# Kernel tuning notes

Hardware: AMD Instinct MI355X
Metric: run time of the kernel (lower is better)

Reference implementation:

```python
import jax, jax.numpy as jnp
import numpy as np

N, E, G = 40000, 640000, 64
D, H, O = 128, 128, 10
EPS = 1e-5


def _lin(k, fan_in, shape):
    b = 1.0 / np.sqrt(fan_in)
    return jax.random.uniform(k, shape, jnp.float32, -b, b)


def setup_inputs() -> dict:
    key = jax.random.key(0)
    ks = jax.random.split(key, 12)
    x = jax.random.normal(ks[0], (N, D), jnp.float32)
    edge_index = jax.random.randint(ks[1], (2, E), 0, N)
    batch = jnp.sort(jax.random.randint(ks[2], (N,), 0, G))
    return {
        "x": x,
        "edge_index": edge_index,
        "batch": batch,
        "num_graphs": G,
        "W_gcn": _lin(ks[3], D, (D, H)),
        "b_gcn": jnp.zeros((H,), jnp.float32),
        "gamma": jnp.ones((H,), jnp.float32),
        "beta": jnp.zeros((H,), jnp.float32),
        "W1": _lin(ks[4], 3 * H, (3 * H, H)),
        "b1": _lin(ks[5], 3 * H, (H,)),
        "W2": _lin(ks[6], H, (H, H // 2)),
        "b2": _lin(ks[7], H, (H // 2,)),
        "W3": _lin(ks[8], H // 2, (H // 2, O)),
        "b3": _lin(ks[9], H // 2, (O,)),
    }


def reference(x, edge_index, batch, num_graphs, W_gcn, b_gcn, gamma, beta, W1, b1, W2, b2, W3, b3):
    n = x.shape[0]
    src, dst = edge_index[0], edge_index[1]
    # GCNConv: h = D^{-1/2} (A + I) D^{-1/2} (x W) + b  (self-loops, symmetric norm)
    h = x @ W_gcn                                   # [N, H]
    deg = jax.ops.segment_sum(jnp.ones((src.shape[0],), h.dtype), dst, num_segments=n) + 1.0
    dinv = jax.lax.rsqrt(deg)                       # [N]
    coef = dinv[src] * dinv[dst]                    # [E]
    msg = h[src] * coef[:, None]                    # [E, H] gather (memory bound)
    agg = jax.ops.segment_sum(msg, dst, num_segments=n)
    agg = agg + h * (dinv * dinv)[:, None] + b_gcn  # self-loop term + bias
    h = jax.nn.relu(agg)
    # LayerNorm over feature dim
    mu = jnp.mean(h, axis=-1, keepdims=True)
    var = jnp.mean(jnp.square(h - mu), axis=-1, keepdims=True)
    h = (h - mu) * jax.lax.rsqrt(var + EPS) * gamma + beta
    # global mean / add / max pools keyed by graph id
    counts = jax.ops.segment_sum(jnp.ones((n,), h.dtype), batch, num_segments=num_graphs)
    x_add = jax.ops.segment_sum(h, batch, num_segments=num_graphs)
    x_mean = x_add / jnp.maximum(counts, 1.0)[:, None]
    x_max = jax.ops.segment_max(h, batch, num_segments=num_graphs)
    x_max = jnp.where(counts[:, None] > 0, x_max, 0.0)
    g = jnp.concatenate([x_mean, x_add, x_max], axis=1)  # [G, 3H]
    # MLP head (dropout is identity at inference)
    g = jax.nn.relu(g @ W1 + b1)
    g = jax.nn.relu(g @ W2 + b2)
    return g @ W3 + b3
```

## Files before the change

### kernel.cpp

```cpp
#include <hip/hip_runtime.h>
#include <math.h>

#define EPS 1e-5f
#define FLT_BIG 3.402823466e38f

typedef __attribute__((ext_vector_type(8))) short bf16x8;
typedef __attribute__((ext_vector_type(4))) float f32x4;

__device__ __forceinline__ unsigned fflip(float f){
  int i = __float_as_int(f);
  return (unsigned)(i ^ ((i>>31) | 0x80000000));
}
__device__ __forceinline__ float funflip(unsigned u){
  int i = (u & 0x80000000u) ? (int)(u ^ 0x80000000u) : (int)(~u);
  return __int_as_float(i);
}
__device__ __forceinline__ unsigned f2bf(float f){
  unsigned u = __float_as_uint(f);
  return (u + 0x7FFFu + ((u>>16)&1u)) >> 16;
}
__device__ __forceinline__ float bf_lo(unsigned v){ return __uint_as_float(v<<16); }
__device__ __forceinline__ float bf_hi(unsigned v){ return __uint_as_float(v & 0xFFFF0000u); }

__device__ __forceinline__ int lbound(const int* __restrict__ a, int n, int key){
  int lo=0, hi=n;
  while(lo<hi){ int mid=(lo+hi)>>1; if(a[mid]<key) lo=mid+1; else hi=mid; }
  return lo;
}

__global__ __launch_bounds__(256) void k_bucketize(
    const int* __restrict__ src, const int* __restrict__ dst, int E, int NB,
    unsigned* __restrict__ gcur, unsigned* __restrict__ dstream,
    const float* __restrict__ Wg, ushort* __restrict__ Wp,
    const int* __restrict__ batch, int N, int* __restrict__ gcnt, int G){
  __shared__ unsigned whist[4][160];
  __shared__ unsigned hist[160];
  __shared__ unsigned excl[160];
  __shared__ unsigned base[160];
  __shared__ unsigned wsum[4];
  __shared__ unsigned lsorted[2048];
  int t = threadIdx.x, bid = blockIdx.x;
  int wid = t>>6, lane = t&63;

  if(bid < 8){
    int i = bid*256 + t;
    int tile = i>>6, l = i&63;
    int kt = tile>>3, ct = tile&7;
    int q = l>>4, nn = l&15;
    ushort w8[8];
    #pragma unroll
    for(int j=0;j<8;j++)
      w8[j] = (ushort)f2bf(Wg[(kt*32 + q*8 + j)*128 + ct*16 + nn]);
    ushort* dstp = Wp + (size_t)i*8;
    #pragma unroll
    for(int j=0;j<8;j++) dstp[j] = w8[j];
  } else if(bid == 8){
    if(t < G){
      int s = lbound(batch,N,t), e = lbound(batch,N,t+1);
      gcnt[t] = e - s;
    }
  }

  int e0 = bid*2048 + t*8;
  unsigned rec[8]; int bk[8]; unsigned rr[8];
  #pragma unroll
  for(int j=0;j<8;j++) bk[j] = -1;
  if(e0+7 < E){
    int4 s0 = *(const int4*)(src+e0), s1 = *(const int4*)(src+e0+4);
    int4 d0 = *(const int4*)(dst+e0), d1 = *(const int4*)(dst+e0+4);
    int ss[8] = {s0.x,s0.y,s0.z,s0.w,s1.x,s1.y,s1.z,s1.w};
    int dd[8] = {d0.x,d0.y,d0.z,d0.w,d1.x,d1.y,d1.z,d1.w};
    #pragma unroll
    for(int j=0;j<8;j++){
      bk[j] = dd[j]>>8;
      rec[j] = ((unsigned)bk[j]<<24) | ((unsigned)(dd[j]&255)<<16) | (unsigned)ss[j];
    }
  } else {
    #pragma unroll
    for(int j=0;j<8;j++){
      int ee = e0+j;
      if(ee<E){
        int s = src[ee], d = dst[ee];
        bk[j] = d>>8;
        rec[j] = ((unsigned)bk[j]<<24) | ((unsigned)(d&255)<<16) | (unsigned)s;
      }
    }
  }
  for(int i=t;i<NB;i+=256){
    whist[0][i]=0u; whist[1][i]=0u; whist[2][i]=0u; whist[3][i]=0u;
  }
  __syncthreads();
  #pragma unroll
  for(int j=0;j<8;j++)
    if(bk[j]>=0) rr[j] = atomicAdd(&whist[wid][bk[j]],1u);
  __syncthreads();
  unsigned hv = 0u;
  if(t<NB){
    unsigned h0=whist[0][t], h1=whist[1][t], h2=whist[2][t], h3=whist[3][t];
    hv = h0+h1+h2+h3;
    hist[t] = hv;
    whist[0][t]=0u; whist[1][t]=h0; whist[2][t]=h0+h1; whist[3][t]=h0+h1+h2;
  }
  unsigned v = hv;
  #pragma unroll
  for(int d=1; d<64; d<<=1){
    unsigned o = __shfl_up(v, d, 64);
    if(lane >= d) v += o;
  }
  if(lane==63) wsum[wid] = v;
  __syncthreads();
  {
    unsigned pre = 0;
    if(wid>0) pre += wsum[0];
    if(wid>1) pre += wsum[1];
    if(wid>2) pre += wsum[2];
    if(t<NB) excl[t] = v + pre - hv;
  }
  if(t<NB){
    int ridx = t + bid; while(ridx>=NB) ridx-=NB;
    base[ridx] = atomicAdd(&gcur[ridx], hist[ridx]);
  }
  __syncthreads();
  #pragma unroll
  for(int j=0;j<8;j++)
    if(bk[j]>=0) lsorted[excl[bk[j]] + whist[wid][bk[j]] + rr[j]] = rec[j];
  __syncthreads();
  int vc = E - bid*2048; if(vc>2048) vc=2048;
  #pragma unroll
  for(int j=0;j<8;j++){
    int k = j*256 + t;
    if(k<vc){
      unsigned rc = lsorted[k];
      unsigned bb = rc>>24;
      unsigned pos = base[bb] + (unsigned)k - excl[bb];
      if(pos < 8192u) dstream[((size_t)bb<<13) + pos] = rc;
    }
  }
}

__global__ __launch_bounds__(1024) void k_csrscale(
    const unsigned* __restrict__ dstream, const unsigned* __restrict__ gcur,
    int N, ushort* __restrict__ csr, int* __restrict__ cursor,
    const float4* __restrict__ x4, uint2* __restrict__ xs2){
  __shared__ unsigned cnt[256];
  __shared__ float dv[256];
  __shared__ ushort slab[16384];
  int b = blockIdx.x, t = threadIdx.x;
  if(t<256) cnt[t]=0u;
  {
    unsigned sv = ((unsigned)N<<16) | (unsigned)N;
    uint4 fillv = make_uint4(sv,sv,sv,sv);
    #pragma unroll
    for(int i=t;i<2048;i+=1024) ((uint4*)slab)[i] = fillv;
  }
  if(b==0 && t<16) ((uint4*)(xs2 + ((size_t)N<<5)))[t] = make_uint4(0,0,0,0);
  __syncthreads();
  int nb = (int)gcur[b]; if(nb>8192) nb=8192;
  const unsigned* sp = dstream + ((size_t)b<<13);
  for(int i=t;i<nb;i+=1024){
    unsigned rc = sp[i];
    int dl = (rc>>16)&255;
    unsigned p = atomicAdd(&cnt[dl],1u);
    if(p<64u) slab[(dl<<6)+(int)p] = (ushort)(rc & 0xFFFFu);
  }
  __syncthreads();
  const uint4* s4 = (const uint4*)slab;
  uint4* c4 = ((uint4*)csr) + ((size_t)b<<11);
  #pragma unroll
  for(int i=t;i<2048;i+=1024) c4[i] = s4[i];
  if(t<256){
    int node = (b<<8) + t;
    if(node<N) cursor[node] = (int)cnt[t];
    int deg = (int)cnt[t]; if(deg>64) deg=64;
    dv[t] = rsqrtf((float)deg + 1.0f);
  }
  __syncthreads();
  int base = b<<8;
  for(int i=t; i<8192; i+=1024){
    int nl = i>>5;
    int node = base + nl;
    if(node<N){
      float dinv = dv[nl];
      size_t idx = ((size_t)node<<5) + (i&31);
      float4 v = x4[idx];
      uint2 o;
      o.x = (f2bf(v.y*dinv)<<16) | f2bf(v.x*dinv);
      o.y = (f2bf(v.w*dinv)<<16) | f2bf(v.z*dinv);
      xs2[idx] = o;
    }
  }
}

__global__ void k_agg(const uint4* __restrict__ xs4, const int* __restrict__ cursor,
                      const ushort* __restrict__ csr, int n, uint4* __restrict__ zb4){
  int w = (blockIdx.x*blockDim.x + threadIdx.x)>>6;
  if(w>=n) return;
  int lane = threadIdx.x & 63;
  int grp = lane>>4, li = lane&15;
  int deg = cursor[w]; if(deg>64) deg=64;
  int k0 = w<<6;
  float dd = rsqrtf((float)deg + 1.0f);
  float a0=0.f,a1=0.f,a2=0.f,a3=0.f,a4=0.f,a5=0.f,a6=0.f,a7=0.f;
  if(grp==0){
    uint4 sv = xs4[(w<<4)+li];
    a0=bf_lo(sv.x); a1=bf_hi(sv.x); a2=bf_lo(sv.y); a3=bf_hi(sv.y);
    a4=bf_lo(sv.z); a5=bf_hi(sv.z); a6=bf_lo(sv.w); a7=bf_hi(sv.w);
  }
  for(int kb=0; kb<deg; kb+=16){
    int base = k0 + kb + (grp<<2);
    ushort4 s4 = *(const ushort4*)(csr + base);
    { uint4 v = xs4[((int)s4.x<<4)+li];
      a0+=bf_lo(v.x); a1+=bf_hi(v.x); a2+=bf_lo(v.y); a3+=bf_hi(v.y);
      a4+=bf_lo(v.z); a5+=bf_hi(v.z); a6+=bf_lo(v.w); a7+=bf_hi(v.w); }
    { uint4 v = xs4[((int)s4.y<<4)+li];
      a0+=bf_lo(v.x); a1+=bf_hi(v.x); a2+=bf_lo(v.y); a3+=bf_hi(v.y);
      a4+=bf_lo(v.z); a5+=bf_hi(v.z); a6+=bf_lo(v.w); a7+=bf_hi(v.w); }
    { uint4 v = xs4[((int)s4.z<<4)+li];
      a0+=bf_lo(v.x); a1+=bf_hi(v.x); a2+=bf_lo(v.y); a3+=bf_hi(v.y);
      a4+=bf_lo(v.z); a5+=bf_hi(v.z); a6+=bf_lo(v.w); a7+=bf_hi(v.w); }
    { uint4 v = xs4[((int)s4.w<<4)+li];
      a0+=bf_lo(v.x); a1+=bf_hi(v.x); a2+=bf_lo(v.y); a3+=bf_hi(v.y);
      a4+=bf_lo(v.z); a5+=bf_hi(v.z); a6+=bf_lo(v.w); a7+=bf_hi(v.w); }
  }
  a0 += __shfl_xor(a0,16,64); a1 += __shfl_xor(a1,16,64);
  a2 += __shfl_xor(a2,16,64); a3 += __shfl_xor(a3,16,64);
  a4 += __shfl_xor(a4,16,64); a5 += __shfl_xor(a5,16,64);
  a6 += __shfl_xor(a6,16,64); a7 += __shfl_xor(a7,16,64);
  a0 += __shfl_xor(a0,32,64); a1 += __shfl_xor(a1,32,64);
  a2 += __shfl_xor(a2,32,64); a3 += __shfl_xor(a3,32,64);
  a4 += __shfl_xor(a4,32,64); a5 += __shfl_xor(a5,32,64);
  a6 += __shfl_xor(a6,32,64); a7 += __shfl_xor(a7,32,64);
  if(grp==0){
    uint4 o;
    o.x = (f2bf(a1*dd)<<16) | f2bf(a0*dd);
    o.y = (f2bf(a3*dd)<<16) | f2bf(a2*dd);
    o.z = (f2bf(a5*dd)<<16) | f2bf(a4*dd);
    o.w = (f2bf(a7*dd)<<16) | f2bf(a6*dd);
    zb4[(w<<4)+li] = o;
  }
}

__global__ __launch_bounds__(256) void k_gemmln(
    const unsigned* __restrict__ zb, const ushort* __restrict__ Wp,
    const float* __restrict__ bgc, const float* __restrict__ gamma, const float* __restrict__ beta,
    const int* __restrict__ batch, int n,
    float* __restrict__ pool_sum, unsigned* __restrict__ pool_maxu){
  __shared__ float sred[4][128];
  __shared__ float mred[4][128];
  int t = threadIdx.x, lane = t & 63, wv = t >> 6;
  int rowBase = blockIdx.x*64;
  int q = lane>>4, nn = lane&15;
  int m = rowBase + wv*16 + nn;
  bf16x8 afr[4];
  if(m < n){
    const char* rp = (const char*)zb + (size_t)m*256;
    #pragma unroll
    for(int kt=0;kt<4;kt++)
      afr[kt] = *(const bf16x8*)(rp + kt*64 + q*16);
  } else {
    #pragma unroll
    for(int kt=0;kt<4;kt++) afr[kt] = (bf16x8){0,0,0,0,0,0,0,0};
  }

  f32x4 acc[8];
  #pragma unroll
  for(int ct=0;ct<8;ct++){
    f32x4 c = {0.f,0.f,0.f,0.f};
    #pragma unroll
    for(int kt=0;kt<4;kt++){
      bf16x8 bfr = *(const bf16x8*)(Wp + ((size_t)(kt*8+ct)*64 + lane)*8);
      c = __builtin_amdgcn_mfma_f32_16x16x32_bf16(afr[kt], bfr, c, 0, 0, 0);
    }
    acc[ct] = c;
  }
  float s[4]={0,0,0,0}, qq[4]={0,0,0,0};
  #pragma unroll
  for(int ct=0;ct<8;ct++){
    float bb = bgc[ct*16+nn];
    #pragma unroll
    for(int r=0;r<4;r++){
      float v = acc[ct][r] + bb;
      v = fmaxf(v, 0.f);
      acc[ct][r] = v;
      s[r] += v; qq[r] += v*v;
    }
  }
  #pragma unroll
  for(int d=1; d<16; d<<=1){
    #pragma unroll
    for(int r=0;r<4;r++){
      s[r]  += __shfl_xor(s[r],  d, 64);
      qq[r] += __shfl_xor(qq[r], d, 64);
    }
  }
  float mu[4], isd[4];
  #pragma unroll
  for(int r=0;r<4;r++){
    mu[r] = s[r]*(1.f/128.f);
    float var = qq[r]*(1.f/128.f) - mu[r]*mu[r];
    isd[r] = rsqrtf(var + EPS);
  }
  #pragma unroll
  for(int ct=0;ct<8;ct++){
    float gm = gamma[ct*16+nn], bt = beta[ct*16+nn];
    #pragma unroll
    for(int r=0;r<4;r++)
      acc[ct][r] = (acc[ct][r]-mu[r])*isd[r]*gm + bt;
  }
  int gbr[4];
  #pragma unroll
  for(int r=0;r<4;r++){
    int gr = rowBase + wv*16 + q*4 + r;
    gbr[r] = (gr < n) ? batch[gr] : -1;
  }
  int b0i = rowBase; if(b0i >= n) b0i = n-1;
  int b63i = rowBase + 63; if(b63i >= n) b63i = n-1;
  int gmin = batch[b0i], gmax = batch[b63i];
  if(gmax < gmin) gmax = gmin;
  for(int g=gmin; g<=gmax; ++g){
    #pragma unroll
    for(int ct=0;ct<8;ct++){
      float ssum = 0.f, smax = -FLT_BIG;
      #pragma unroll
      for(int r=0;r<4;r++){
        if(gbr[r]==g){
          ssum += acc[ct][r];
          smax = fmaxf(smax, acc[ct][r]);
        }
      }
      ssum += __shfl_xor(ssum, 16, 64);
      ssum += __shfl_xor(ssum, 32, 64);
      float o1 = __shfl_xor(smax, 16, 64); smax = fmaxf(smax, o1);
      float o2 = __shfl_xor(smax, 32, 64); smax = fmaxf(smax, o2);
      if(q==0){
        sred[wv][ct*16+nn] = ssum;
        mred[wv][ct*16+nn] = smax;
      }
    }
    __syncthreads();
    if(t < 128){
      float s0 = (sred[0][t]+sred[1][t]) + (sred[2][t]+sred[3][t]);
      float m0 = fmaxf(fmaxf(mred[0][t],mred[1][t]), fmaxf(mred[2][t],mred[3][t]));
      if(s0 != 0.f)    atomicAdd(&pool_sum[g*128 + t], s0);
      if(m0 > -FLT_BIG) atomicMax(&pool_maxu[g*128 + t], fflip(m0));
    }
    __syncthreads();
  }
}

__global__ __launch_bounds__(512) void k_head(
    const float* __restrict__ pool_sum, const unsigned* __restrict__ pool_maxu,
    const int* __restrict__ gcnt,
    const float* __restrict__ W1, const float* __restrict__ b1,
    const float* __restrict__ W2, const float* __restrict__ b2,
    const float* __restrict__ W3, const float* __restrict__ b3,
    float* __restrict__ out){
  int g = blockIdx.x, t = threadIdx.x;
  __shared__ float red[4][128];
  __shared__ float gl[384];
  __shared__ float h1[128];
  __shared__ float h2[64];
  int cnt = gcnt[g];
  if(t<384){
    int j = t & 127;
    if(t<128){
      gl[t] = pool_sum[g*128+j] / (float)((cnt>1)?cnt:1);
    } else if(t<256){
      gl[t] = pool_sum[g*128+j];
    } else {
      float m = funflip(pool_maxu[g*128+j]);
      gl[t] = (cnt>0) ? m : 0.f;
    }
  }
  __syncthreads();
  int j = t & 127, kh = t >> 7;
  float p=0.f;
  for(int k=kh*96; k<kh*96+96; k++) p += gl[k]*W1[k*128+j];
  red[kh][j]=p;
  __syncthreads();
  if(t<128){
    float v = red[0][t]+red[1][t]+red[2][t]+red[3][t]+b1[t];
    h1[t]=fmaxf(v,0.f);
  }
  __syncthreads();
  if(t<64){
    float a=b2[t];
    for(int k=0;k<128;k++) a += h1[k]*W2[k*64+t];
    h2[t]=fmaxf(a,0.f);
  }
  __syncthreads();
  if(t<10){
    float a=b3[t];
    for(int k=0;k<64;k++) a += h2[k]*W3[k*10+t];
    out[g*10+t]=a;
  }
}

extern "C" void kernel_launch(void* const* d_in, const int* in_sizes, int n_in,
                              void* d_out, int out_size, void* d_ws, size_t ws_size,
                              hipStream_t stream){
  const float* x     = (const float*)d_in[0];
  const int*   ei    = (const int*)d_in[1];
  const int*   batch = (const int*)d_in[2];
  const float* Wg    = (const float*)d_in[4];
  const float* bg    = (const float*)d_in[5];
  const float* gamma = (const float*)d_in[6];
  const float* beta  = (const float*)d_in[7];
  const float* W1    = (const float*)d_in[8];
  const float* b1    = (const float*)d_in[9];
  const float* W2    = (const float*)d_in[10];
  const float* b2    = (const float*)d_in[11];
  const float* W3    = (const float*)d_in[12];
  const float* b3    = (const float*)d_in[13];
  float* out = (float*)d_out;

  int N = in_sizes[0]/128;
  int E = in_sizes[1]/2;
  const int G = 64;
  const int* src = ei;
  const int* dst = ei + E;
  int NB = (N+255)>>8;

  char* p = (char*)d_ws;
  auto alloc=[&](size_t bytes)->char*{ char* r=p; p += (bytes+255)&~(size_t)255; return r; };
  size_t zr_bytes = (size_t)G*128*4 + (size_t)G*128*4 + 1024;
  char*     zr      = alloc(zr_bytes);
  float*    psum    = (float*)zr;
  unsigned* pmaxu   = (unsigned*)(zr + (size_t)G*128*4);
  unsigned* gcur    = (unsigned*)(zr + (size_t)G*128*4*2);
  int*      cursor  = (int*)     alloc((size_t)N*4);
  ushort*   csr     = (ushort*)  alloc((size_t)NB*16384*2);
  unsigned* zb      = (unsigned*)alloc((size_t)N*64*4);
  unsigned* xs      = (unsigned*)alloc((size_t)(N+1)*64*4);
  ushort*   Wp      = (ushort*)  alloc(2048*8*2);
  int*      gcnt    = (int*)     alloc((size_t)G*4);
  unsigned* dstream = (unsigned*)alloc((size_t)NB*8192*4);

  hipMemsetAsync(zr, 0, zr_bytes, stream);
  int bb = (E+2047)/2048;
  k_bucketize<<<bb,256,0,stream>>>(src,dst,E,NB,gcur,dstream,Wg,Wp,batch,N,gcnt,G);
  k_csrscale<<<NB,1024,0,stream>>>(dstream,gcur,N,csr,cursor,(const float4*)x,(uint2*)xs);
  int ab = (int)(((size_t)N*64 + 255)/256);
  k_agg<<<ab,256,0,stream>>>((const uint4*)xs,cursor,csr,N,(uint4*)zb);
  k_gemmln<<<(N+63)/64,256,0,stream>>>(zb,Wp,bg,gamma,beta,batch,N,psum,pmaxu);
  k_head<<<G,512,0,stream>>>(psum,pmaxu,gcnt,W1,b1,W2,b2,W3,b3,out);
}
```

Measured before the change: 156.8 us.

## Fuse MLP head into gemmln via last-block-per-graph completion counter

Removes the separate k_head launch. Each graph's pooled features are finalized by whichever gemmln block finishes last for that graph, which it detects with a per-graph atomic done counter and an expected block count computed in bucketize. That block then runs the three-layer MLP head in place. This saves one kernel launch and its tail, at the cost of extra shared memory and serial head work inside a few gemmln blocks. Correctness depends on gblk matching the gemmln loop's per-block graph iteration.

```diff
diff --git a/kernel.cpp b/kernel.cpp
--- a/kernel.cpp
+++ b/kernel.cpp
@@ -32,7 +32,8 @@
     const int* __restrict__ src, const int* __restrict__ dst, int E, int NB,
     unsigned* __restrict__ gcur, unsigned* __restrict__ dstream,
     const float* __restrict__ Wg, ushort* __restrict__ Wp,
-    const int* __restrict__ batch, int N, int* __restrict__ gcnt, int G){
+    const int* __restrict__ batch, int N, int* __restrict__ gcnt,
+    int* __restrict__ gblk, int G){
   __shared__ unsigned whist[4][160];
   __shared__ unsigned hist[160];
   __shared__ unsigned excl[160];
@@ -58,6 +59,7 @@
     if(t < G){
       int s = lbound(batch,N,t), e = lbound(batch,N,t+1);
       gcnt[t] = e - s;
+      gblk[t] = (e > s) ? (((e-1)>>6) - (s>>6) + 1) : 0;
     }
   }
 
@@ -244,9 +246,20 @@
     const unsigned* __restrict__ zb, const ushort* __restrict__ Wp,
     const float* __restrict__ bgc, const float* __restrict__ gamma, const float* __restrict__ beta,
     const int* __restrict__ batch, int n,
-    float* __restrict__ pool_sum, unsigned* __restrict__ pool_maxu){
+    float* __restrict__ pool_sum, unsigned* __restrict__ pool_maxu,
+    const int* __restrict__ gcnt, const int* __restrict__ gblk,
+    unsigned* __restrict__ gdone,
+    const float* __restrict__ W1, const float* __restrict__ b1,
+    const float* __restrict__ W2, const float* __restrict__ b2,
+    const float* __restrict__ W3, const float* __restrict__ b3,
+    float* __restrict__ out){
   __shared__ float sred[4][128];
   __shared__ float mred[4][128];
+  __shared__ float gl[384];
+  __shared__ float hred[2][128];
+  __shared__ float h1[128];
+  __shared__ float h2[64];
+  __shared__ int trig_s;
   int t = threadIdx.x, lane = t & 63, wv = t >> 6;
   int rowBase = blockIdx.x*64;
   int q = lane>>4, nn = lane&15;
@@ -345,54 +358,43 @@
       if(m0 > -FLT_BIG) atomicMax(&pool_maxu[g*128 + t], fflip(m0));
     }
     __syncthreads();
-  }
-}
-
-__global__ __launch_bounds__(512) void k_head(
-    const float* __restrict__ pool_sum, const unsigned* __restrict__ pool_maxu,
-    const int* __restrict__ gcnt,
-    const float* __restrict__ W1, const float* __restrict__ b1,
-    const float* __restrict__ W2, const float* __restrict__ b2,
-    const float* __restrict__ W3, const float* __restrict__ b3,
-    float* __restrict__ out){
-  int g = blockIdx.x, t = threadIdx.x;
-  __shared__ float red[4][128];
-  __shared__ float gl[384];
-  __shared__ float h1[128];
-  __shared__ float h2[64];
-  int cnt = gcnt[g];
-  if(t<384){
-    int j = t & 127;
-    if(t<128){
-      gl[t] = pool_sum[g*128+j] / (float)((cnt>1)?cnt:1);
-    } else if(t<256){
-      gl[t] = pool_sum[g*128+j];
-    } else {
-      float m = funflip(pool_maxu[g*128+j]);
-      gl[t] = (cnt>0) ? m : 0.f;
-    }
-  }
-  __syncthreads();
-  int j = t & 127, kh = t >> 7;
-  float p=0.f;
-  for(int k=kh*96; k<kh*96+96; k++) p += gl[k]*W1[k*128+j];
-  red[kh][j]=p;
-  __syncthreads();
-  if(t<128){
-    float v = red[0][t]+red[1][t]+red[2][t]+red[3][t]+b1[t];
-    h1[t]=fmaxf(v,0.f);
-  }
-  __syncthreads();
-  if(t<64){
-    float a=b2[t];
-    for(int k=0;k<128;k++) a += h1[k]*W2[k*64+t];
-    h2[t]=fmaxf(a,0.f);
-  }
-  __syncthreads();
-  if(t<10){
-    float a=b3[t];
-    for(int k=0;k<64;k++) a += h2[k]*W3[k*10+t];
-    out[g*10+t]=a;
+    if(t==0){
+      __threadfence();
+      unsigned old = atomicAdd(&gdone[g], 1u);
+      trig_s = (old == (unsigned)(gblk[g]-1));
+    }
+    __syncthreads();
+    if(trig_s){
+      int cnt = gcnt[g];
+      float rinv = 1.f/(float)((cnt>1)?cnt:1);
+      if(t<128){
+        float sv = atomicAdd(&pool_sum[g*128+t], 0.f);
+        gl[t]     = sv*rinv;
+        gl[128+t] = sv;
+        unsigned mu_ = atomicOr(&pool_maxu[g*128+t], 0u);
+        gl[256+t] = (cnt>0) ? funflip(mu_) : 0.f;
+      }
+      __syncthreads();
+      int j = t & 127, kh = t >> 7;
+      float p = 0.f;
+      for(int k=kh*192; k<kh*192+192; k++) p += gl[k]*W1[k*128+j];
+      hred[kh][j] = p;
+      __syncthreads();
+      if(t<128) h1[t] = fmaxf(hred[0][t]+hred[1][t]+b1[t], 0.f);
+      __syncthreads();
+      if(t<64){
+        float a = b2[t];
+        for(int k=0;k<128;k++) a += h1[k]*W2[k*64+t];
+        h2[t] = fmaxf(a, 0.f);
+      }
+      __syncthreads();
+      if(t<10){
+        float a = b3[t];
+        for(int k=0;k<64;k++) a += h2[k]*W3[k*10+t];
+        out[g*10+t] = a;
+      }
+    }
+    __syncthreads();
   }
 }
 
@@ -423,25 +425,27 @@
 
   char* p = (char*)d_ws;
   auto alloc=[&](size_t bytes)->char*{ char* r=p; p += (bytes+255)&~(size_t)255; return r; };
-  size_t zr_bytes = (size_t)G*128*4 + (size_t)G*128*4 + 1024;
+  size_t zr_bytes = (size_t)G*128*4*2 + 1024 + 1024;
   char*     zr      = alloc(zr_bytes);
   float*    psum    = (float*)zr;
   unsigned* pmaxu   = (unsigned*)(zr + (size_t)G*128*4);
   unsigned* gcur    = (unsigned*)(zr + (size_t)G*128*4*2);
+  unsigned* gdone   = (unsigned*)(zr + (size_t)G*128*4*2 + 1024);
   int*      cursor  = (int*)     alloc((size_t)N*4);
   ushort*   csr     = (ushort*)  alloc((size_t)NB*16384*2);
   unsigned* zb      = (unsigned*)alloc((size_t)N*64*4);
   unsigned* xs      = (unsigned*)alloc((size_t)(N+1)*64*4);
   ushort*   Wp      = (ushort*)  alloc(2048*8*2);
   int*      gcnt    = (int*)     alloc((size_t)G*4);
+  int*      gblk    = (int*)     alloc((size_t)G*4);
   unsigned* dstream = (unsigned*)alloc((size_t)NB*8192*4);
 
   hipMemsetAsync(zr, 0, zr_bytes, stream);
   int bb = (E+2047)/2048;
-  k_bucketize<<<bb,256,0,stream>>>(src,dst,E,NB,gcur,dstream,Wg,Wp,batch,N,gcnt,G);
+  k_bucketize<<<bb,256,0,stream>>>(src,dst,E,NB,gcur,dstream,Wg,Wp,batch,N,gcnt,gblk,G);
   k_csrscale<<<NB,1024,0,stream>>>(dstream,gcur,N,csr,cursor,(const float4*)x,(uint2*)xs);
   int ab = (int)(((size_t)N*64 + 255)/256);
   k_agg<<<ab,256,0,stream>>>((const uint4*)xs,cursor,csr,N,(uint4*)zb);
-  k_gemmln<<<(N+63)/64,256,0,stream>>>(zb,Wp,bg,gamma,beta,batch,N,psum,pmaxu);
-  k_head<<<G,512,0,stream>>>(psum,pmaxu,gcnt,W1,b1,W2,b2,W3,b3,out);
-}
+  k_gemmln<<<(N+63)/64,256,0,stream>>>(zb,Wp,bg,gamma,beta,batch,N,psum,pmaxu,
+                                       gcnt,gblk,gdone,W1,b1,W2,b2,W3,b3,out);
+}
```

Measured after the change: 171.9 us. +9.6%, slower.
